# Kernel optimization log

Hardware: AMD Instinct MI355X
Metric: run time of the kernel (lower is better)

## Reference

```python
import jax, jax.numpy as jnp
import numpy as np

D_MODEL = 256      # num_nodes == d_model (forced by pre_relation mask shape)
MW = 2             # moving_window (hardcoded '2' in MPNN reshape)
STRIDE = 1
DECAY = 0.7
INPUT_DIM = 64
OUTPUT_DIM = 64
BN_EPS = 1e-5


def _mask_matrix():
    # Mask_Matrix: block (i,j) of size d_model x d_model equals decay**|i-j|
    blocks = DECAY ** np.abs(np.arange(MW)[:, None] - np.arange(MW)[None, :])
    return jnp.asarray(np.kron(blocks, np.ones((D_MODEL, D_MODEL))).astype(np.float32))


def _bn(h, w, b):
    # training-mode BatchNorm1d over channel-last layout [B, N, C]
    mu = h.mean(axis=(0, 1))
    var = h.var(axis=(0, 1))  # biased variance, as torch uses for normalization
    return (h - mu) * jax.lax.rsqrt(var + BN_EPS) * w + b


def setup_inputs() -> dict:
    key = jax.random.key(0)
    ks = jax.random.split(key, 4)
    bs, scale_num = 16, 17
    x = jax.random.normal(ks[0], (bs, scale_num, D_MODEL, INPUT_DIM), jnp.float32)
    # mapping2 weights scaled small to keep the dot-product softmax well conditioned
    w_map2 = jax.random.normal(ks[1], (INPUT_DIM, INPUT_DIM), jnp.float32) * 0.05
    b_map2 = jnp.zeros((INPUT_DIM,), jnp.float32)
    bn0_w = jnp.ones((INPUT_DIM,), jnp.float32)
    bn0_b = jnp.zeros((INPUT_DIM,), jnp.float32)
    th0_w = jax.random.normal(ks[2], (OUTPUT_DIM, INPUT_DIM), jnp.float32) / np.float32(np.sqrt(INPUT_DIM))
    th0_b = jnp.zeros((OUTPUT_DIM,), jnp.float32)
    th1_w = jax.random.normal(ks[3], (OUTPUT_DIM, INPUT_DIM), jnp.float32) / np.float32(np.sqrt(INPUT_DIM))
    th1_b = jnp.zeros((OUTPUT_DIM,), jnp.float32)
    bn1_w = jnp.ones((OUTPUT_DIM,), jnp.float32)
    bn1_b = jnp.zeros((OUTPUT_DIM,), jnp.float32)
    return dict(x=x, w_map2=w_map2, b_map2=b_map2, bn0_w=bn0_w, bn0_b=bn0_b,
                th0_w=th0_w, th0_b=th0_b, th1_w=th1_w, th1_b=th1_b,
                bn1_w=bn1_w, bn1_b=bn1_b)


def reference(x, w_map2, b_map2, bn0_w, bn0_b, th0_w, th0_b, th1_w, th1_b, bn1_w, bn1_b):
    bs, S, N, F = x.shape
    L = (S - MW) // STRIDE + 1  # num_windows from F.unfold
    # WindowConv_Graph + transpose(2,3) + reshape: X[b,l,m,n,f] = x[b, l*stride+m, n, f]
    idx = np.arange(L)[:, None] * STRIDE + np.arange(MW)[None, :]
    X = x[:, idx].reshape(bs * L, MW * N, F)  # [B', N1, F]

    # Dot_Graph_Construction_weights (N1 != d_model -> mapping2 branch)
    nf = X @ w_map2.T + b_map2                       # [B', N1, F]
    adj = jnp.einsum('bnf,bmf->bnm', nf, nf)         # [B', N1, N1]
    eye = jnp.eye(MW * N, dtype=x.dtype)
    adj = jax.nn.leaky_relu(adj - eye * 1e8)
    adj = jax.nn.softmax(adj, axis=-1) + eye

    # decay mask multiply
    adj = adj * _mask_matrix()

    # BatchNorm over input_dim channels
    xb = _bn(nf, bn0_w, bn0_b)

    # MPNN_mk_v2, field=2, way='sum'
    out = (adj @ xb) @ th0_w.T + th0_b               # hop 1
    adj2 = adj @ adj
    out = out + (adj2 @ xb) @ th1_w.T + th1_b        # hop 2
    out = jax.nn.leaky_relu(_bn(out, bn1_w, bn1_b))

    # pooling over the moving_window axis (mean), then over windows (mean)
    out = out.reshape(bs, L, MW, N, OUTPUT_DIM).mean(axis=2)
    return out.mean(axis=1)  # [bs, num_nodes, output_dim]
```

## Files before the change

kernel.cpp:

```cpp
#include <hip/hip_runtime.h>


typedef unsigned short u16;
typedef __bf16 bf16x8 __attribute__((ext_vector_type(8)));
typedef float f32x4 __attribute__((ext_vector_type(4)));
typedef unsigned int u32x4 __attribute__((ext_vector_type(4)));

#define MFMA16(a, b, c) __builtin_amdgcn_mfma_f32_16x16x32_bf16(a, b, c, 0, 0, 0)

#define BSZ 16
#define SNUM 17
#define FD 64
#define NB 256
#define N1 512
#define SL_ELEMS 16384
#define Y_ELEMS (BSZ * SNUM * SL_ELEMS)

#define WM_O 0
#define BM_O 4096
#define B0W_O 4160
#define B0B_O 4224
#define T0W_O 4288
#define T0B_O 8384
#define T1W_O 8448
#define T1B_O 12544
#define B1W_O 12608
#define B1B_O 12672
#define P_TOT 12736

#define SLAB2_O 32768
#define RED_O 65536
#define SCR_O 65792
#define LDS_BYTES ((SCR_O + 16 * 640) * 2)

__device__ __forceinline__ float bf2f(u16 u) {
    union { unsigned int i; float f; } v;
    v.i = ((unsigned int)u) << 16;
    return v.f;
}
__device__ __forceinline__ u16 f2bu(float f) {
    __bf16 h = (__bf16)f;
    return __builtin_bit_cast(u16, h);
}
__device__ __forceinline__ u16 f2bf(float f) {
    unsigned int u = __builtin_bit_cast(unsigned int, f);
    unsigned int r = (u + 0x7fffu + ((u >> 16) & 1u)) >> 16;
    return (u16)r;
}
__device__ __forceinline__ bf16x8 ld8g(const u16* p) {
    return __builtin_bit_cast(bf16x8, *reinterpret_cast<const u32x4*>(p));
}

__global__ __launch_bounds__(256) void k_prep(
    const void* p0, const void* p1, const void* p2, const void* p3,
    const void* p4, const void* p5, const void* p6, const void* p7,
    const void* p8, const void* p9, int* __restrict__ flagOut,
    u16* __restrict__ pc, float* __restrict__ stats) {
    const int tid = threadIdx.x, lane = tid & 63;
    int z = 0, bc = 0;
    const unsigned int* w = (const unsigned int*)p0;
    for (int i = lane; i < 2048; i += 64) {
        const unsigned int v = w[i];
        z += ((v & 0xffffu) == 0u);
        bc += (v >> 14) & 1;
    }
#pragma unroll
    for (int o = 1; o < 64; o <<= 1) {
        z += __shfl_xor(z, o);
        bc += __shfl_xor(bc, o);
    }
    const int flag = (z > 1024 || bc > 256) ? 1 : 0;
    if (blockIdx.x == 0) {
        if (tid == 0) *flagOut = flag;
        if (tid < 256) stats[tid] = 0.f;
    }
    const int i = blockIdx.x * 256 + tid;
    if (i >= P_TOT) return;
    const void* src;
    int si;
    if (i < BM_O)        { src = p0; si = i; }
    else if (i < B0W_O)  { src = p1; si = i - BM_O; }
    else if (i < B0B_O)  { src = p2; si = i - B0W_O; }
    else if (i < T0W_O)  { src = p3; si = i - B0B_O; }
    else if (i < T0B_O)  { src = p4; si = i - T0W_O; }
    else if (i < T1W_O)  { src = p5; si = i - T0B_O; }
    else if (i < T1B_O)  { src = p6; si = i - T1W_O; }
    else if (i < B1W_O)  { src = p7; si = i - T1B_O; }
    else if (i < B1B_O)  { src = p8; si = i - B1W_O; }
    else                 { src = p9; si = i - B1B_O; }
    pc[i] = flag ? f2bf(((const float*)src)[si]) : ((const u16*)src)[si];
}

__global__ __launch_bounds__(256) void k_y(const void* __restrict__ xv,
                                           const int* __restrict__ flag,
                                           const u16* __restrict__ pc,
                                           u16* __restrict__ y,
                                           float* __restrict__ gstats) {
    const int slice = blockIdx.x;
    const int tid = threadIdx.x, wave = tid >> 6, lane = tid & 63;
    const int quad = lane >> 4, l16 = lane & 15;
    __shared__ float red[128];
    if (tid < 128) red[tid] = 0.f;
    const int isf32 = *flag;

    f32x4 acc[4][4];
#pragma unroll
    for (int i = 0; i < 4; i++)
#pragma unroll
        for (int j = 0; j < 4; j++) acc[i][j] = (f32x4){0.f, 0.f, 0.f, 0.f};

    bf16x8 bfr[4][2];
#pragma unroll
    for (int nt = 0; nt < 4; nt++)
#pragma unroll
        for (int kh = 0; kh < 2; kh++)
            bfr[nt][kh] = ld8g(pc + WM_O + (nt * 16 + l16) * 64 + kh * 32 + quad * 8);

    const float* xf = (const float*)xv + (size_t)slice * SL_ELEMS;
    const u16* xh = (const u16*)xv + (size_t)slice * SL_ELEMS;

#pragma unroll
    for (int mt = 0; mt < 4; mt++) {
        const int row = wave * 64 + mt * 16 + l16;
        bf16x8 a0, a1;
        if (isf32) {
            const float* r0 = xf + row * 64 + quad * 8;
            f32x4 v0 = *(const f32x4*)r0;
            f32x4 v1 = *(const f32x4*)(r0 + 4);
            f32x4 v2 = *(const f32x4*)(r0 + 32);
            f32x4 v3 = *(const f32x4*)(r0 + 36);
#pragma unroll
            for (int j = 0; j < 4; j++) {
                a0[j] = (__bf16)v0[j]; a0[4 + j] = (__bf16)v1[j];
                a1[j] = (__bf16)v2[j]; a1[4 + j] = (__bf16)v3[j];
            }
        } else {
            a0 = ld8g(xh + row * 64 + quad * 8);
            a1 = ld8g(xh + row * 64 + 32 + quad * 8);
        }
#pragma unroll
        for (int nt = 0; nt < 4; nt++)
            acc[mt][nt] = MFMA16(a1, bfr[nt][1], MFMA16(a0, bfr[nt][0], acc[mt][nt]));
    }

    u16* ys = y + (size_t)slice * SL_ELEMS;
    float s1[4] = {0.f, 0.f, 0.f, 0.f}, s2[4] = {0.f, 0.f, 0.f, 0.f};
#pragma unroll
    for (int nt = 0; nt < 4; nt++) {
        const int col = nt * 16 + l16;
        const float bias = bf2f(pc[BM_O + col]);
#pragma unroll
        for (int mt = 0; mt < 4; mt++)
#pragma unroll
            for (int r = 0; r < 4; r++) {
                const int row = wave * 64 + mt * 16 + quad * 4 + r;
                const float v = acc[mt][nt][r] + bias;
                ys[row * 64 + col] = f2bu(v);
                s1[nt] += v;
                s2[nt] += v * v;
            }
        s1[nt] += __shfl_xor(s1[nt], 16); s1[nt] += __shfl_xor(s1[nt], 32);
        s2[nt] += __shfl_xor(s2[nt], 16); s2[nt] += __shfl_xor(s2[nt], 32);
    }
    __syncthreads();
    if (quad == 0) {
#pragma unroll
        for (int nt = 0; nt < 4; nt++) {
            atomicAdd(&red[nt * 16 + l16], s1[nt]);
            atomicAdd(&red[64 + nt * 16 + l16], s2[nt]);
        }
    }
    __syncthreads();
    const int s = slice % SNUM;
    const float wgt = (s == 0 || s == SNUM - 1) ? 1.f : 2.f;
    if (tid < 128) atomicAdd(&gstats[tid], red[tid] * wgt);
}

__global__ __launch_bounds__(1024) void k_mega(
    const u16* __restrict__ y, float* __restrict__ stats,
    const u16* __restrict__ pc, u16* __restrict__ opre) {
    extern __shared__ u16 lds[];
    u16* slab1 = lds;
    u16* slab2 = lds + SLAB2_O;
    float* red = (float*)(lds + RED_O);
    const int tid = threadIdx.x, w = tid >> 6, lane = tid & 63;
    const int quad = lane >> 4, l16 = lane & 15;
    u16* scr = lds + SCR_O + w * 640;
    const int p = blockIdx.x, b = p >> 4, l = p & 15;
    const f32x4 ZERO4 = (f32x4){0.f, 0.f, 0.f, 0.f};

    if (tid < 128) red[tid] = 0.f;

    const float cinv = 1.f / 131072.f;
    const int fme = tid & 63;
    float mu0 = stats[fme] * cinv;
    float vr0 = fmaxf(stats[64 + fme] * cinv - mu0 * mu0, 0.f);
    const float scale_f = rsqrtf(vr0 + 1e-5f) * bf2f(pc[B0W_O + fme]);
    const float shift_f = bf2f(pc[B0B_O + fme]) - mu0 * scale_f;

    const u16* ybase = y + (size_t)(b * SNUM + l) * SL_ELEMS;
#pragma unroll
    for (int i = 0; i < 4; i++) {
        const int gid = i * 1024 + tid, n = gid >> 3, g = gid & 7;
        *(u32x4*)(slab1 + n * 64 + ((g ^ (n & 7)) << 3)) =
            *(const u32x4*)(ybase + n * 64 + g * 8);
    }
    __syncthreads();

#pragma unroll
    for (int i = 0; i < 4; i++) {
        const int gn = (tid >> 6) + i * 16;
        union { u16 u[8]; u32x4 v; } pk;
#pragma unroll
        for (int j = 0; j < 8; j++) {
            const int n = gn * 8 + j;
            const u16 raw = slab1[n * 64 + (((fme >> 3) ^ (n & 7)) << 3) + (fme & 7)];
            pk.u[j] = f2bu(bf2f(raw) * scale_f + shift_f);
        }
        *(u32x4*)(slab2 + fme * 512 + ((gn ^ fme) << 3)) = pk.v;
    }
    __syncthreads();

    bf16x8 a[2][2];
#pragma unroll
    for (int st = 0; st < 2; st++)
#pragma unroll
        for (int h = 0; h < 2; h++) {
            const int row = w * 32 + st * 16 + l16;
            a[st][h] = *(const bf16x8*)(slab1 + row * 64 + (((h * 4 + quad) ^ (row & 7)) << 3));
        }

    for (int pass = 0; pass < 2; pass++) {
        f32x4 oacc[2][4];
        f32x4 lsum[2];
#pragma unroll
        for (int st = 0; st < 2; st++) {
            lsum[st] = ZERO4;
#pragma unroll
            for (int ft = 0; ft < 4; ft++) oacc[st][ft] = ZERO4;
        }

        for (int c = 0; c < 8; c++) {
            const float mf = ((w >= 8) == (c >= 4)) ? 1.f : 0.7f;
#pragma unroll
            for (int ch = 0; ch < 2; ch++) {
                bf16x8 bs[2][2], bv[4];
#pragma unroll
                for (int jt = 0; jt < 2; jt++)
#pragma unroll
                    for (int h = 0; h < 2; h++) {
                        const int rj = c * 64 + ch * 32 + jt * 16 + l16;
                        bs[jt][h] = *(const bf16x8*)(slab1 + rj * 64 + (((h * 4 + quad) ^ (rj & 7)) << 3));
                    }
#pragma unroll
                for (int ft = 0; ft < 4; ft++) {
                    const int f = ft * 16 + l16, gn = c * 8 + ch * 4 + quad;
                    bv[ft] = *(const bf16x8*)(slab2 + f * 512 + ((gn ^ f) << 3));
                }
                const int colbase = c * 64 + ch * 32;
#pragma unroll
                for (int st = 0; st < 2; st++) {
                    f32x4 S[2];
#pragma unroll
                    for (int jt = 0; jt < 2; jt++) {
                        f32x4 t = MFMA16(a[st][0], bs[jt][0], ZERO4);
                        S[jt] = MFMA16(a[st][1], bs[jt][1], t);
                    }
                    const int rowbase = w * 32 + st * 16;
#pragma unroll
                    for (int jt = 0; jt < 2; jt++)
#pragma unroll
                        for (int r = 0; r < 4; r++) {
                            const float s = S[jt][r];
                            const float m2 = s > 0.f ? 1.44269504f : 0.0144269504f;
                            float pv = exp2f(fminf(s * m2, 86.f));
                            if (colbase + jt * 16 == rowbase && l16 == quad * 4 + r) pv = 0.f;
                            lsum[st][r] += pv;
                            scr[(quad * 4 + r) * 40 + jt * 16 + l16] = f2bu(pv * mf);
                        }
                    const bf16x8 pa = *(const bf16x8*)(scr + l16 * 40 + quad * 8);
#pragma unroll
                    for (int ft = 0; ft < 4; ft++)
                        oacc[st][ft] = MFMA16(pa, bv[ft], oacc[st][ft]);
                }
            }
        }
#pragma unroll
        for (int st = 0; st < 2; st++)
#pragma unroll
            for (int r = 0; r < 4; r++) {
                lsum[st][r] += __shfl_xor(lsum[st][r], 1);
                lsum[st][r] += __shfl_xor(lsum[st][r], 2);
                lsum[st][r] += __shfl_xor(lsum[st][r], 4);
                lsum[st][r] += __shfl_xor(lsum[st][r], 8);
            }

        if (pass == 0) {
#pragma unroll
            for (int st = 0; st < 2; st++) {
                f32x4 inv;
#pragma unroll
                for (int r = 0; r < 4; r++) inv[r] = __builtin_amdgcn_rcpf(lsum[st][r]);
#pragma unroll
                for (int ft = 0; ft < 4; ft++)
#pragma unroll
                    for (int r = 0; r < 4; r++) {
                        const int i = w * 32 + st * 16 + quad * 4 + r;
                        const int f = ft * 16 + l16;
                        const float xbv = bf2f(slab2[f * 512 + (((i >> 3) ^ f) << 3) + (i & 7)]);
                        oacc[st][ft][r] = oacc[st][ft][r] * inv[r] + xbv;
                    }
            }
            __syncthreads();
#pragma unroll
            for (int st = 0; st < 2; st++)
#pragma unroll
                for (int ft = 0; ft < 4; ft++)
#pragma unroll
                    for (int r = 0; r < 4; r++) {
                        const int i = w * 32 + st * 16 + quad * 4 + r;
                        const int f = ft * 16 + l16;
                        slab2[f * 512 + (((i >> 3) ^ f) << 3) + (i & 7)] = f2bu(oacc[st][ft][r]);
                    }
            __syncthreads();
        } else {
            float s1a[4] = {0.f, 0.f, 0.f, 0.f}, s2a[4] = {0.f, 0.f, 0.f, 0.f};
#pragma unroll
            for (int st = 0; st < 2; st++) {
                f32x4 inv;
#pragma unroll
                for (int r = 0; r < 4; r++) inv[r] = __builtin_amdgcn_rcpf(lsum[st][r]);
#pragma unroll
                for (int ft = 0; ft < 4; ft++)
#pragma unroll
                    for (int r = 0; r < 4; r++) {
                        const int i = w * 32 + st * 16 + quad * 4 + r;
                        const int f = ft * 16 + l16;
                        const float o1 = bf2f(slab2[f * 512 + (((i >> 3) ^ f) << 3) + (i & 7)]);
                        oacc[st][ft][r] = oacc[st][ft][r] * inv[r] + o1;
                    }
                bf16x8 a1[2], a2[2];
                const int irow = w * 32 + st * 16 + l16;
#pragma unroll
                for (int h = 0; h < 2; h++)
#pragma unroll
                    for (int j = 0; j < 8; j++) {
                        const int f = h * 32 + quad * 8 + j;
                        const u16 raw = slab2[f * 512 + (((irow >> 3) ^ f) << 3) + (irow & 7)];
                        a1[h][j] = __builtin_bit_cast(__bf16, raw);
                    }
#pragma unroll
                for (int h = 0; h < 2; h++) {
#pragma unroll
                    for (int ftl = 0; ftl < 2; ftl++)
#pragma unroll
                        for (int r = 0; r < 4; r++)
                            scr[(quad * 4 + r) * 40 + ftl * 16 + l16] = f2bu(oacc[st][2 * h + ftl][r]);
                    a2[h] = *(const bf16x8*)(scr + l16 * 40 + quad * 8);
                }
                f32x4 pacc[4];
#pragma unroll
                for (int ot = 0; ot < 4; ot++) {
                    const int o = ot * 16 + l16;
                    const float bias = bf2f(pc[T0B_O + o]) + bf2f(pc[T1B_O + o]);
                    pacc[ot] = (f32x4){bias, bias, bias, bias};
                }
#pragma unroll
                for (int h = 0; h < 2; h++)
#pragma unroll
                    for (int ot = 0; ot < 4; ot++) {
                        const int o = ot * 16 + l16;
                        bf16x8 w0f = ld8g(pc + T0W_O + o * 64 + h * 32 + quad * 8);
                        bf16x8 w1f = ld8g(pc + T1W_O + o * 64 + h * 32 + quad * 8);
                        pacc[ot] = MFMA16(a1[h], w0f, pacc[ot]);
                        pacc[ot] = MFMA16(a2[h], w1f, pacc[ot]);
                    }
#pragma unroll
                for (int ot = 0; ot < 4; ot++)
#pragma unroll
                    for (int r = 0; r < 4; r++) {
                        const int i = w * 32 + st * 16 + quad * 4 + r;
                        const int o = ot * 16 + l16;
                        const float v = pacc[ot][r];
                        s1a[ot] += v;
                        s2a[ot] += v * v;
                        opre[(size_t)p * (N1 * FD) + (size_t)i * 64 + o] = f2bu(v);
                    }
            }
#pragma unroll
            for (int ot = 0; ot < 4; ot++) {
                s1a[ot] += __shfl_xor(s1a[ot], 16); s1a[ot] += __shfl_xor(s1a[ot], 32);
                s2a[ot] += __shfl_xor(s2a[ot], 16); s2a[ot] += __shfl_xor(s2a[ot], 32);
            }
            if (quad == 0) {
#pragma unroll
                for (int ot = 0; ot < 4; ot++) {
                    atomicAdd(&red[ot * 16 + l16], s1a[ot]);
                    atomicAdd(&red[64 + ot * 16 + l16], s2a[ot]);
                }
            }
            __syncthreads();
            if (tid < 128) atomicAdd(&stats[128 + tid], red[tid]);
        }
    }
}

__global__ __launch_bounds__(256) void k_final(const u16* __restrict__ op,
                                               const float* __restrict__ stats,
                                               const u16* __restrict__ pc,
                                               float* __restrict__ out) {
    const int o = blockIdx.x * 256 + threadIdx.x;
    const int f = o & 63, n = (o >> 6) & 255, b = o >> 14;
    const float inv = 1.f / 131072.f;
    const float mu = stats[128 + f] * inv;
    const float var = fmaxf(stats[192 + f] * inv - mu * mu, 0.f);
    const float rs = rsqrtf(var + 1e-5f);
    const float scale = rs * bf2f(pc[B1W_O + f]);
    const float shift = bf2f(pc[B1B_O + f]) - mu * scale;
    float acc = 0.f;
    for (int l = 0; l < 16; l++) {
        const size_t pb = (size_t)(b * 16 + l) * N1 * FD;
#pragma unroll
        for (int m = 0; m < 2; m++) {
            float v = bf2f(op[pb + (size_t)(m * 256 + n) * 64 + f]);
            v = v * scale + shift;
            acc += (v > 0.f ? v : 0.01f * v);
        }
    }
    out[o] = acc * (1.f / 32.f);
}

extern "C" void kernel_launch(void* const* d_in, const int* in_sizes, int n_in,
                              void* d_out, int out_size, void* d_ws, size_t ws_size,
                              hipStream_t stream) {
    char* ws = (char*)d_ws;
    size_t off = 0;
    auto alloc = [&](size_t bytes) { void* pp = ws + off; off += (bytes + 255) & ~(size_t)255; return pp; };
    u16* y = (u16*)alloc((size_t)Y_ELEMS * 2);
    u16* opre = (u16*)alloc((size_t)NB * N1 * FD * 2);
    u16* pc = (u16*)alloc(P_TOT * 2);
    float* stats = (float*)alloc(256 * 4);
    int* flag = (int*)alloc(256);
    float* out = (float*)d_out;

    k_prep<<<50, 256, 0, stream>>>(d_in[1], d_in[2], d_in[3], d_in[4], d_in[5],
                                   d_in[6], d_in[7], d_in[8], d_in[9], d_in[10],
                                   flag, pc, stats);
    k_y<<<BSZ * SNUM, 256, 0, stream>>>(d_in[0], flag, pc, y, stats);
    k_mega<<<NB, 1024, LDS_BYTES, stream>>>(y, stats, pc, opre);
    k_final<<<1024, 256, 0, stream>>>(opre, stats, pc, out);
}
```

Before: 203.7 us.

## Compute softmax row sums via MFMA and reload operands from LDS to cut registers

The per-lane scalar accumulation of softmax row sums and the final cross-lane shuffle reduction are replaced by an extra MFMA that multiplies the probability tile by a constant vector (1 or 1/0.7 to undo the decay factor). The persistent A-operand registers and the prefetched B/V operands are dropped and reloaded from LDS right where they are used, lowering register pressure. The cost is more LDS traffic and one extra MFMA per tile. The row sums are now taken from bf16-rounded values, which slightly changes normalization accuracy.

```diff
diff --git a/kernel.cpp b/kernel.cpp
--- a/kernel.cpp
+++ b/kernel.cpp
@@ -198,6 +198,13 @@
     const float scale_f = rsqrtf(vr0 + 1e-5f) * bf2f(pc[B0W_O + fme]);
     const float shift_f = bf2f(pc[B0B_O + fme]) - mu0 * scale_f;
 
+    bf16x8 rbA, rbB;
+#pragma unroll
+    for (int j = 0; j < 8; j++) {
+        rbA[j] = (__bf16)1.0f;
+        rbB[j] = (__bf16)1.4285715f;
+    }
+
     const u16* ybase = y + (size_t)(b * SNUM + l) * SL_ELEMS;
 #pragma unroll
     for (int i = 0; i < 4; i++) {
@@ -221,15 +228,6 @@
     }
     __syncthreads();
 
-    bf16x8 a[2][2];
-#pragma unroll
-    for (int st = 0; st < 2; st++)
-#pragma unroll
-        for (int h = 0; h < 2; h++) {
-            const int row = w * 32 + st * 16 + l16;
-            a[st][h] = *(const bf16x8*)(slab1 + row * 64 + (((h * 4 + quad) ^ (row & 7)) << 3));
-        }
-
     for (int pass = 0; pass < 2; pass++) {
         f32x4 oacc[2][4];
         f32x4 lsum[2];
@@ -241,32 +239,27 @@
         }
 
         for (int c = 0; c < 8; c++) {
-            const float mf = ((w >= 8) == (c >= 4)) ? 1.f : 0.7f;
+            const bool same = ((w >= 8) == (c >= 4));
+            const float mf = same ? 1.f : 0.7f;
+            const bf16x8 rb = same ? rbA : rbB;
 #pragma unroll
             for (int ch = 0; ch < 2; ch++) {
-                bf16x8 bs[2][2], bv[4];
-#pragma unroll
-                for (int jt = 0; jt < 2; jt++)
-#pragma unroll
-                    for (int h = 0; h < 2; h++) {
-                        const int rj = c * 64 + ch * 32 + jt * 16 + l16;
-                        bs[jt][h] = *(const bf16x8*)(slab1 + rj * 64 + (((h * 4 + quad) ^ (rj & 7)) << 3));
-                    }
-#pragma unroll
-                for (int ft = 0; ft < 4; ft++) {
-                    const int f = ft * 16 + l16, gn = c * 8 + ch * 4 + quad;
-                    bv[ft] = *(const bf16x8*)(slab2 + f * 512 + ((gn ^ f) << 3));
-                }
                 const int colbase = c * 64 + ch * 32;
 #pragma unroll
                 for (int st = 0; st < 2; st++) {
+                    const int rowbase = w * 32 + st * 16;
+                    const int arow = rowbase + l16;
+                    const bf16x8 a0 = *(const bf16x8*)(slab1 + arow * 64 + ((quad ^ (arow & 7)) << 3));
+                    const bf16x8 a1 = *(const bf16x8*)(slab1 + arow * 64 + (((4 + quad) ^ (arow & 7)) << 3));
                     f32x4 S[2];
 #pragma unroll
                     for (int jt = 0; jt < 2; jt++) {
-                        f32x4 t = MFMA16(a[st][0], bs[jt][0], ZERO4);
-                        S[jt] = MFMA16(a[st][1], bs[jt][1], t);
-                    }
-                    const int rowbase = w * 32 + st * 16;
+                        const int rj = colbase + jt * 16 + l16;
+                        const bf16x8 b0 = *(const bf16x8*)(slab1 + rj * 64 + ((quad ^ (rj & 7)) << 3));
+                        const bf16x8 b1 = *(const bf16x8*)(slab1 + rj * 64 + (((4 + quad) ^ (rj & 7)) << 3));
+                        f32x4 t = MFMA16(a0, b0, ZERO4);
+                        S[jt] = MFMA16(a1, b1, t);
+                    }
 #pragma unroll
                     for (int jt = 0; jt < 2; jt++)
 #pragma unroll
@@ -275,25 +268,19 @@
                             const float m2 = s > 0.f ? 1.44269504f : 0.0144269504f;
                             float pv = exp2f(fminf(s * m2, 86.f));
                             if (colbase + jt * 16 == rowbase && l16 == quad * 4 + r) pv = 0.f;
-                            lsum[st][r] += pv;
                             scr[(quad * 4 + r) * 40 + jt * 16 + l16] = f2bu(pv * mf);
                         }
                     const bf16x8 pa = *(const bf16x8*)(scr + l16 * 40 + quad * 8);
-#pragma unroll
-                    for (int ft = 0; ft < 4; ft++)
-                        oacc[st][ft] = MFMA16(pa, bv[ft], oacc[st][ft]);
+                    lsum[st] = MFMA16(pa, rb, lsum[st]);
+#pragma unroll
+                    for (int ft = 0; ft < 4; ft++) {
+                        const int f = ft * 16 + l16, gn = c * 8 + ch * 4 + quad;
+                        const bf16x8 bv = *(const bf16x8*)(slab2 + f * 512 + ((gn ^ f) << 3));
+                        oacc[st][ft] = MFMA16(pa, bv, oacc[st][ft]);
+                    }
                 }
             }
         }
-#pragma unroll
-        for (int st = 0; st < 2; st++)
-#pragma unroll
-            for (int r = 0; r < 4; r++) {
-                lsum[st][r] += __shfl_xor(lsum[st][r], 1);
-                lsum[st][r] += __shfl_xor(lsum[st][r], 2);
-                lsum[st][r] += __shfl_xor(lsum[st][r], 4);
-                lsum[st][r] += __shfl_xor(lsum[st][r], 8);
-            }
 
         if (pass == 0) {
 #pragma unroll
```

New measurement: 204.6 us. About the same (+0.4%).
